# Optimization experiments

Measured on AMD Instinct MI355X. Metric: run time of the kernel, lower is better.

The kernel has to match this reference:

```python
import jax, jax.numpy as jnp
import numpy as np

T, N, E, D, H, L = 8, 50000, 800000, 128, 128, 2


def setup_inputs() -> dict:
    key = jax.random.key(0)
    ks = jax.random.split(key, 16)
    s = 1.0 / np.sqrt(H)  # glorot-ish scale so gates don't saturate
    inp = {
        "x": jax.random.normal(ks[0], (T, N, D), jnp.float32),
        "h0": jax.random.normal(ks[1], (L, N, H), jnp.float32) * 0.1,
        "edge_index": jax.random.randint(ks[2], (2, E), 0, N, jnp.int32),
    }
    for j, n in enumerate(["Wxz", "Whz", "Wxr", "Whr", "Wxh", "Whh"]):
        inp[n] = jax.random.normal(ks[3 + j], (L, H, H), jnp.float32) * s
    for n in ["bxz", "bhz", "bxr", "bhr", "bxh", "bhh"]:
        inp[n] = jnp.zeros((L, H), jnp.float32)
    return inp


def reference(x, h0, Wxz, Whz, Wxr, Whr, Wxh, Whh,
              bxz, bhz, bxr, bhr, bxh, bhh, edge_index):
    n_nodes = x.shape[1]
    n_layer = h0.shape[0]
    # GCNConv(improved=True): add self-loops with weight 2, symmetric norm.
    loop = jnp.arange(n_nodes, dtype=edge_index.dtype)
    row = jnp.concatenate([edge_index[0], loop])
    col = jnp.concatenate([edge_index[1], loop])
    w = jnp.concatenate([jnp.ones((edge_index.shape[1],), x.dtype),
                         jnp.full((n_nodes,), 2.0, x.dtype)])
    deg = jax.ops.segment_sum(w, row, num_segments=n_nodes)
    dinv = jnp.where(deg > 0, deg ** -0.5, 0.0)
    norm = dinv[row] * w * dinv[col]  # [E+N]

    def gcn(v, W, b):
        # gather -> weight -> scatter-add (identity activation inside GRU)
        m = norm[:, None] * (v @ W)[col]          # [E+N, H]
        return jax.ops.segment_sum(m, row, num_segments=n_nodes) + b

    def step(h, xt):
        hs = []
        inp = xt
        for i in range(n_layer):
            z = jax.nn.sigmoid(gcn(inp, Wxz[i], bxz[i]) + gcn(h[i], Whz[i], bhz[i]))
            r = jax.nn.sigmoid(gcn(inp, Wxr[i], bxr[i]) + gcn(h[i], Whr[i], bhr[i]))
            h_tilde = jnp.tanh(gcn(inp, Wxh[i], bxh[i]) + gcn(r * h[i], Whh[i], bhh[i]))
            hn = z * h[i] + (1.0 - z) * h_tilde
            hs.append(hn)
            inp = hn
        h_new = jnp.stack(hs)
        return h_new, h_new[-1]

    _, hs_top = jax.lax.scan(step, h0, x)  # [T, N, H] top-layer states
    return hs_top
```

## Files before the change

kernel.cpp:

```cpp
#include <hip/hip_runtime.h>
#include <hip/hip_fp16.h>

#define TT 8
#define NN 50000
#define EE 800000
#define HH 128
#define LL 2

typedef __attribute__((ext_vector_type(8))) short short8_t;
typedef __attribute__((ext_vector_type(4))) float f32x4;

__device__ __forceinline__ float bf2f(unsigned short b){ return __uint_as_float(((unsigned)b)<<16); }
__device__ __forceinline__ unsigned short f2bf(float f){
  unsigned u = __float_as_uint(f);
  u += 0x7fffu + ((u>>16)&1u);
  return (unsigned short)(u>>16);
}
__device__ __forceinline__ float fin(float v){
  return (v == v && fabsf(v) < 1e30f) ? v : 0.0f;
}
__device__ __forceinline__ float sigm(float x){ return 1.0f/(1.0f+__expf(-x)); }
__device__ __forceinline__ float tanh_fast(float x){
  float t = __expf(-2.0f*fabsf(x));
  float r = (1.0f-t)/(1.0f+t);
  return copysignf(r,x);
}

__global__ void k_detect(const unsigned short* __restrict__ xr, int* __restrict__ flag){
  __shared__ int sm[256];
  int bad = 0;
  for (int i = threadIdx.x; i < 4096; i += 256){
    float v = bf2f(xr[i]);
    if (!(fabsf(v) < 64.0f)) bad++;
  }
  sm[threadIdx.x] = bad; __syncthreads();
  for (int off=128; off>0; off>>=1){
    if (threadIdx.x < off) sm[threadIdx.x] += sm[threadIdx.x+off];
    __syncthreads();
  }
  if (threadIdx.x == 0) flag[0] = (sm[0] > 8) ? 1 : 0;
}

__global__ void k_hist(const int* __restrict__ row, int* __restrict__ counts, int E){
  int e = blockIdx.x*256 + threadIdx.x;
  if (e < E){
    int r = row[e];
    if ((unsigned)r < (unsigned)NN) atomicAdd(&counts[r], 1);
  }
}
__global__ void k_dinv(const int* __restrict__ counts, float* __restrict__ dinv, int N){
  int i = blockIdx.x*256 + threadIdx.x;
  if (i < N) dinv[i] = rsqrtf((float)counts[i] + 2.0f);
}
__global__ void k_reduce(const int* __restrict__ counts, int* __restrict__ part, int N){
  __shared__ int sm[256];
  int i = blockIdx.x*256 + threadIdx.x;
  sm[threadIdx.x] = (i < N) ? counts[i] : 0;
  __syncthreads();
  for (int off=128; off>0; off>>=1){
    if (threadIdx.x < off) sm[threadIdx.x] += sm[threadIdx.x+off];
    __syncthreads();
  }
  if (threadIdx.x == 0) part[blockIdx.x] = sm[0];
}
__global__ void k_scan_partials(const int* __restrict__ part, int* __restrict__ pscan,
                                int nb, int* __restrict__ rowptr, int N, int E){
  __shared__ int sm[256];
  int t = threadIdx.x;
  int v = (t < nb) ? part[t] : 0;
  sm[t] = v; __syncthreads();
  for (int off=1; off<256; off<<=1){
    int x = (t >= off) ? sm[t-off] : 0;
    __syncthreads();
    sm[t] += x;
    __syncthreads();
  }
  if (t < nb) pscan[t] = sm[t] - v;
  if (t == 0) rowptr[N] = E;
}
__global__ void k_scan_final(const int* __restrict__ counts, const int* __restrict__ pscan,
                             int* __restrict__ rowptr, int* __restrict__ cursor, int N){
  __shared__ int sm[256];
  int t = threadIdx.x;
  int i = blockIdx.x*256 + t;
  int v = (i < N) ? counts[i] : 0;
  sm[t] = v; __syncthreads();
  for (int off=1; off<256; off<<=1){
    int x = (t >= off) ? sm[t-off] : 0;
    __syncthreads();
    sm[t] += x;
    __syncthreads();
  }
  int ex = sm[t] - v + pscan[blockIdx.x];
  if (i < N){ rowptr[i] = ex; cursor[i] = ex; }
}
__global__ void k_fill(const int* __restrict__ row, const int* __restrict__ col,
                       int* __restrict__ cursor, const float* __restrict__ dinv,
                       int* __restrict__ colss, float* __restrict__ wsrc, int E){
  int e = blockIdx.x*256 + threadIdx.x;
  if (e < E){
    int r = row[e];
    if ((unsigned)r >= (unsigned)NN) return;
    int p = atomicAdd(&cursor[r], 1);
    if ((unsigned)p >= (unsigned)EE) return;
    int c = col[e];
    if ((unsigned)c >= (unsigned)NN) c = 0;
    colss[p] = c;
    wsrc[p] = dinv[c];
  }
}
__global__ void k_h0(const void* __restrict__ h0, float* __restrict__ h,
                     const int* __restrict__ flag, int n){
  const int fl = *flag;
  int i = blockIdx.x*256 + threadIdx.x;
  if (i < n){
    float v = fl ? ((const float*)h0)[i] : bf2f(((const unsigned short*)h0)[i]);
    h[i] = fin(v);
  }
}
__global__ void k_transpose(const void* W0, const void* W1, const void* W2,
                            const void* W3, const void* W4, const void* W5,
                            unsigned short* __restrict__ Wt_hi,
                            unsigned short* __restrict__ Wt_lo,
                            const int* __restrict__ flag){
  const int fl = *flag;
  int mat = blockIdx.y;
  int wsel = mat >> 1, l = mat & 1;
  const void* W;
  switch (wsel){
    case 0: W = W0; break; case 1: W = W1; break; case 2: W = W2; break;
    case 3: W = W3; break; case 4: W = W4; break; default: W = W5; break;
  }
  int idx = blockIdx.x*256 + threadIdx.x;
  int n = idx >> 7, k = idx & 127;
  size_t src = (size_t)l*16384 + (size_t)k*128 + n;
  float v = fl ? ((const float*)W)[src] : bf2f(((const unsigned short*)W)[src]);
  v = fin(v);
  unsigned short hi = f2bf(v);
  unsigned short lo = f2bf(v - bf2f(hi));
  Wt_hi[(size_t)mat*16384 + idx] = hi;
  Wt_lo[(size_t)mat*16384 + idx] = lo;
}

__global__ __launch_bounds__(256) void gemm_zr(
    const void* __restrict__ S1, long s1_off, int s1_is_x,
    const float* __restrict__ S2,
    const unsigned short* __restrict__ Wz0, const unsigned short* __restrict__ Wz1,
    const unsigned short* __restrict__ Wz2, const unsigned short* __restrict__ Wz3,
    const unsigned short* __restrict__ Wr0, const unsigned short* __restrict__ Wr1,
    const unsigned short* __restrict__ Wr2, const unsigned short* __restrict__ Wr3,
    __half* __restrict__ Cz, __half* __restrict__ Cr,
    int M, const int* __restrict__ flag)
{
  __shared__ short Alds[128*72];
  __shared__ short Bz[128*72];
  __shared__ short Br[128*72];
  const int fl = *flag;
  const int s1bf = s1_is_x && !fl;
  const int nit = fl ? 16 : 8;
  const int tid = threadIdx.x;
  const int m0 = blockIdx.x * 128;

  const int lane = tid & 63;
  const int wid  = tid >> 6;
  const int wm = (wid & 1) << 6;
  const int wn = (wid >> 1) << 6;
  const int lrow = lane & 15;
  const int lk   = (lane >> 4) << 3;

  f32x4 az[4][4], ar[4][4];
#pragma unroll
  for (int i=0;i<4;++i)
#pragma unroll
    for (int j=0;j<4;++j){ az[i][j] = f32x4{0.f,0.f,0.f,0.f}; ar[i][j] = f32x4{0.f,0.f,0.f,0.f}; }

  const int mrow = tid >> 1;
  const int hf   = tid & 1;
  int arow_g = m0 + mrow; if (arow_g >= M) arow_g = M-1;

  for (int it=0; it<nit; ++it){
    const int phase = it >> 2;
    const int k0 = (it & 3) * 32;
    const int koff = k0 + hf*16;
    const bool useS1 = (phase & 1) == 0;
    {
      unsigned pk[16];
      if (useS1 && s1bf){
        const unsigned short* sp = (const unsigned short*)S1 + s1_off + (size_t)arow_g*HH + koff;
        __align__(16) unsigned short tmp[16];
        *(uint4*)&tmp[0] = ((const uint4*)sp)[0];
        *(uint4*)&tmp[8] = ((const uint4*)sp)[1];
#pragma unroll
        for (int j=0;j<16;++j){
          unsigned short t = tmp[j];
          if ((t & 0x7F80u) == 0x7F80u) t = 0;
          pk[j] = (unsigned)t;
        }
      } else {
        __align__(16) float f[16];
        if (useS1){
          const float* sp = (const float*)S1 + s1_off + (size_t)arow_g*HH + koff;
          *(float4*)&f[0]  = ((const float4*)sp)[0];
          *(float4*)&f[4]  = ((const float4*)sp)[1];
          *(float4*)&f[8]  = ((const float4*)sp)[2];
          *(float4*)&f[12] = ((const float4*)sp)[3];
        } else {
          const float* sp = S2 + (size_t)arow_g*HH + koff;
          *(float4*)&f[0]  = ((const float4*)sp)[0];
          *(float4*)&f[4]  = ((const float4*)sp)[1];
          *(float4*)&f[8]  = ((const float4*)sp)[2];
          *(float4*)&f[12] = ((const float4*)sp)[3];
        }
#pragma unroll
        for (int j=0;j<16;++j){
          float v = fin(f[j]);
          unsigned short hi = f2bf(v);
          unsigned short lo = f2bf(v - bf2f(hi));
          pk[j] = (unsigned)hi | ((unsigned)lo << 16);
        }
      }
      short* arp = &Alds[mrow*72 + hf*32];
#pragma unroll
      for (int q=0;q<4;++q){
        uint4 v; v.x=pk[q*4+0]; v.y=pk[q*4+1]; v.z=pk[q*4+2]; v.w=pk[q*4+3];
        *(uint4*)(void*)(arp + q*8) = v;
      }
    }
    {
      const unsigned short* wz = (phase==0) ? Wz0 : (phase==1) ? Wz1 : (phase==2) ? Wz2 : Wz3;
      const unsigned short* wr = (phase==0) ? Wr0 : (phase==1) ? Wr1 : (phase==2) ? Wr2 : Wr3;
      const unsigned short* wpz = wz + (size_t)mrow*HH + koff;
      const unsigned short* wpr = wr + (size_t)mrow*HH + koff;
      __align__(16) unsigned short tz[16], tr[16];
      *(uint4*)&tz[0] = ((const uint4*)wpz)[0];
      *(uint4*)&tz[8] = ((const uint4*)wpz)[1];
      *(uint4*)&tr[0] = ((const uint4*)wpr)[0];
      *(uint4*)&tr[8] = ((const uint4*)wpr)[1];
      short* bzp = &Bz[mrow*72 + hf*32];
      short* brp = &Br[mrow*72 + hf*32];
#pragma unroll
      for (int q=0;q<4;++q){
        uint4 vz, vr;
        vz.x = ((unsigned)tz[q*4+0])*0x00010001u; vz.y = ((unsigned)tz[q*4+1])*0x00010001u;
        vz.z = ((unsigned)tz[q*4+2])*0x00010001u; vz.w = ((unsigned)tz[q*4+3])*0x00010001u;
        vr.x = ((unsigned)tr[q*4+0])*0x00010001u; vr.y = ((unsigned)tr[q*4+1])*0x00010001u;
        vr.z = ((unsigned)tr[q*4+2])*0x00010001u; vr.w = ((unsigned)tr[q*4+3])*0x00010001u;
        *(uint4*)(void*)(bzp + q*8) = vz;
        *(uint4*)(void*)(brp + q*8) = vr;
      }
    }
    __syncthreads();
#pragma unroll
    for (int ks=0; ks<2; ++ks){
      short8_t af[4], bz[4], br[4];
#pragma unroll
      for (int mt=0;mt<4;++mt)
        af[mt] = *(const short8_t*)&Alds[(wm + mt*16 + lrow)*72 + ks*32 + lk];
#pragma unroll
      for (int nt=0;nt<4;++nt){
        bz[nt] = *(const short8_t*)&Bz[(wn + nt*16 + lrow)*72 + ks*32 + lk];
        br[nt] = *(const short8_t*)&Br[(wn + nt*16 + lrow)*72 + ks*32 + lk];
      }
#pragma unroll
      for (int mt=0;mt<4;++mt)
#pragma unroll
        for (int nt=0;nt<4;++nt){
          az[mt][nt] = __builtin_amdgcn_mfma_f32_16x16x32_bf16(af[mt], bz[nt], az[mt][nt], 0, 0, 0);
          ar[mt][nt] = __builtin_amdgcn_mfma_f32_16x16x32_bf16(af[mt], br[nt], ar[mt][nt], 0, 0, 0);
        }
    }
    __syncthreads();
  }
#pragma unroll
  for (int mt=0;mt<4;++mt){
    int rbase = m0 + wm + mt*16 + ((lane>>4)<<2);
#pragma unroll
    for (int nt=0;nt<4;++nt){
      int cc = wn + nt*16 + (lane & 15);
      f32x4 vz = az[mt][nt];
      f32x4 vr = ar[mt][nt];
#pragma unroll
      for (int r=0;r<4;++r){
        int row = rbase + r;
        if (row < M){
          Cz[(size_t)row*HH + cc] = __float2half_rn(vz[r]);
          Cr[(size_t)row*HH + cc] = __float2half_rn(vr[r]);
        }
      }
    }
  }
}

__global__ __launch_bounds__(256) void gemm_h(
    const void* __restrict__ S1, long s1_off, int s1_is_x,
    const __half* __restrict__ S2,
    const unsigned short* __restrict__ W0, const unsigned short* __restrict__ W1,
    const unsigned short* __restrict__ W2, const unsigned short* __restrict__ W3,
    __half* __restrict__ C, int M, const int* __restrict__ flag)
{
  __shared__ short Alds[128*72];
  __shared__ short Blds[128*72];
  const int fl = *flag;
  const int s1bf = s1_is_x && !fl;
  const int nit = fl ? 16 : 8;
  const int tid = threadIdx.x;
  const int m0 = blockIdx.x * 128;

  const int lane = tid & 63;
  const int wid  = tid >> 6;
  const int wm = (wid & 1) << 6;
  const int wn = (wid >> 1) << 6;
  const int lrow = lane & 15;
  const int lk   = (lane >> 4) << 3;

  f32x4 acc[4][4];
#pragma unroll
  for (int i=0;i<4;++i)
#pragma unroll
    for (int j=0;j<4;++j) acc[i][j] = f32x4{0.f,0.f,0.f,0.f};

  const int mrow = tid >> 1;
  const int hf = tid & 1;
  int arow_g = m0 + mrow; if (arow_g >= M) arow_g = M-1;

  for (int it=0; it<nit; ++it){
    const int phase = it >> 2;
    const int k0 = (it & 3) * 32;
    const int koff = k0 + hf*16;
    const bool useS1 = (phase & 1) == 0;
    {
      unsigned pk[16];
      if (useS1 && s1bf){
        const unsigned short* sp = (const unsigned short*)S1 + s1_off + (size_t)arow_g*HH + koff;
        __align__(16) unsigned short tmp[16];
        *(uint4*)&tmp[0] = ((const uint4*)sp)[0];
        *(uint4*)&tmp[8] = ((const uint4*)sp)[1];
#pragma unroll
        for (int j=0;j<16;++j){
          unsigned short t = tmp[j];
          if ((t & 0x7F80u) == 0x7F80u) t = 0;
          pk[j] = (unsigned)t;
        }
      } else {
        __align__(16) float f[16];
        if (useS1){
          const float* sp = (const float*)S1 + s1_off + (size_t)arow_g*HH + koff;
          *(float4*)&f[0]  = ((const float4*)sp)[0];
          *(float4*)&f[4]  = ((const float4*)sp)[1];
          *(float4*)&f[8]  = ((const float4*)sp)[2];
          *(float4*)&f[12] = ((const float4*)sp)[3];
        } else {
          const __half* sp = S2 + (size_t)arow_g*HH + koff;
          __align__(16) __half tmp[16];
          *(uint4*)&tmp[0] = ((const uint4*)sp)[0];
          *(uint4*)&tmp[8] = ((const uint4*)sp)[1];
#pragma unroll
          for (int j=0;j<16;++j) f[j] = __half2float(tmp[j]);
        }
#pragma unroll
        for (int j=0;j<16;++j){
          float v = fin(f[j]);
          unsigned short hi = f2bf(v);
          unsigned short lo = f2bf(v - bf2f(hi));
          pk[j] = (unsigned)hi | ((unsigned)lo << 16);
        }
      }
      short* arp = &Alds[mrow*72 + hf*32];
#pragma unroll
      for (int q=0;q<4;++q){
        uint4 v; v.x=pk[q*4+0]; v.y=pk[q*4+1]; v.z=pk[q*4+2]; v.w=pk[q*4+3];
        *(uint4*)(void*)(arp + q*8) = v;
      }
    }
    {
      const unsigned short* wb = (phase==0) ? W0 : (phase==1) ? W1 : (phase==2) ? W2 : W3;
      const unsigned short* wp = wb + (size_t)mrow*HH + koff;
      __align__(16) unsigned short tb[16];
      *(uint4*)&tb[0] = ((const uint4*)wp)[0];
      *(uint4*)&tb[8] = ((const uint4*)wp)[1];
      unsigned pb[16];
#pragma unroll
      for (int j=0;j<16;++j) pb[j] = ((unsigned)tb[j]) * 0x00010001u;
      short* brp = &Blds[mrow*72 + hf*32];
#pragma unroll
      for (int q=0;q<4;++q){
        uint4 v; v.x=pb[q*4+0]; v.y=pb[q*4+1]; v.z=pb[q*4+2]; v.w=pb[q*4+3];
        *(uint4*)(void*)(brp + q*8) = v;
      }
    }
    __syncthreads();
#pragma unroll
    for (int ks=0; ks<2; ++ks){
      short8_t af[4], bfr[4];
#pragma unroll
      for (int mt=0;mt<4;++mt)
        af[mt] = *(const short8_t*)&Alds[(wm + mt*16 + lrow)*72 + ks*32 + lk];
#pragma unroll
      for (int nt=0;nt<4;++nt)
        bfr[nt] = *(const short8_t*)&Blds[(wn + nt*16 + lrow)*72 + ks*32 + lk];
#pragma unroll
      for (int mt=0;mt<4;++mt)
#pragma unroll
        for (int nt=0;nt<4;++nt)
          acc[mt][nt] = __builtin_amdgcn_mfma_f32_16x16x32_bf16(af[mt], bfr[nt], acc[mt][nt], 0, 0, 0);
    }
    __syncthreads();
  }
#pragma unroll
  for (int mt=0;mt<4;++mt){
    int rbase = m0 + wm + mt*16 + ((lane>>4)<<2);
#pragma unroll
    for (int nt=0;nt<4;++nt){
      int cc = wn + nt*16 + (lane & 15);
      f32x4 a = acc[mt][nt];
#pragma unroll
      for (int r=0;r<4;++r){
        int row = rbase + r;
        if (row < M) C[(size_t)row*HH + cc] = __float2half_rn(a[r]);
      }
    }
  }
}

__global__ __launch_bounds__(256) void prop_zr(
    const __half* __restrict__ Uz, const __half* __restrict__ Ur,
    const int* __restrict__ rowptr, const int* __restrict__ cols,
    const float* __restrict__ wsrc, const float* __restrict__ dinv,
    const void* __restrict__ bxz, const void* __restrict__ bhz,
    const void* __restrict__ bxr, const void* __restrict__ bhr, int boff,
    const float* __restrict__ hl, __half2* __restrict__ zbuf,
    __half2* __restrict__ rhbuf, const int* __restrict__ flag, int N)
{
  const int fl = *flag;
  int lane = threadIdx.x & 63;
  int d = (blockIdx.x << 2) + (threadIdx.x >> 6);
  if (d >= N) return;
  float di = dinv[d];
  const __half2* Uz2 = (const __half2*)Uz;
  const __half2* Ur2 = (const __half2*)Ur;
  float2 az = __half22float2(Uz2[(size_t)d*64 + lane]);
  float2 ar = __half22float2(Ur2[(size_t)d*64 + lane]);
  float sw = 2.0f*di;
  az.x *= sw; az.y *= sw; ar.x *= sw; ar.y *= sw;
  int b = rowptr[d], e = rowptr[d+1];
  if (b < 0) b = 0; if (e > EE) e = EE; if (e < b) e = b;
  for (int base=b; base<e; base+=64){
    int cnt = e - base; if (cnt > 64) cnt = 64;
    int idx = base + lane;
    int mc = (idx < e) ? cols[idx] : 0;
    float mw = (idx < e) ? wsrc[idx] : 0.0f;
    if ((unsigned)mc >= (unsigned)NN){ mc = 0; mw = 0.0f; }
    for (int j=0;j<cnt;++j){
      int s = __shfl(mc, j);
      float w = __shfl(mw, j);
      float2 vz = __half22float2(Uz2[(size_t)s*64 + lane]);
      float2 vr = __half22float2(Ur2[(size_t)s*64 + lane]);
      az.x += w*vz.x; az.y += w*vz.y;
      ar.x += w*vr.x; ar.y += w*vr.y;
    }
  }
  int c = boff + (lane << 1);
  float bxz0 = fl ? ((const float*)bxz)[c]   : bf2f(((const unsigned short*)bxz)[c]);
  float bxz1 = fl ? ((const float*)bxz)[c+1] : bf2f(((const unsigned short*)bxz)[c+1]);
  float bhz0 = fl ? ((const float*)bhz)[c]   : bf2f(((const unsigned short*)bhz)[c]);
  float bhz1 = fl ? ((const float*)bhz)[c+1] : bf2f(((const unsigned short*)bhz)[c+1]);
  float bxr0 = fl ? ((const float*)bxr)[c]   : bf2f(((const unsigned short*)bxr)[c]);
  float bxr1 = fl ? ((const float*)bxr)[c+1] : bf2f(((const unsigned short*)bxr)[c+1]);
  float bhr0 = fl ? ((const float*)bhr)[c]   : bf2f(((const unsigned short*)bhr)[c]);
  float bhr1 = fl ? ((const float*)bhr)[c+1] : bf2f(((const unsigned short*)bhr)[c+1]);
  float z0 = sigm(di*az.x + fin(bxz0) + fin(bhz0));
  float z1 = sigm(di*az.y + fin(bxz1) + fin(bhz1));
  float r0 = sigm(di*ar.x + fin(bxr0) + fin(bhr0));
  float r1 = sigm(di*ar.y + fin(bxr1) + fin(bhr1));
  float2 hv = ((const float2*)hl)[(size_t)d*64 + lane];
  __half2 oz; oz.x = __float2half_rn(z0); oz.y = __float2half_rn(z1);
  __half2 orh; orh.x = __float2half_rn(r0*hv.x); orh.y = __float2half_rn(r1*hv.y);
  zbuf[(size_t)d*64 + lane] = oz;
  rhbuf[(size_t)d*64 + lane] = orh;
}

__global__ __launch_bounds__(256) void prop_h(
    const __half* __restrict__ U, const int* __restrict__ rowptr,
    const int* __restrict__ cols, const float* __restrict__ wsrc,
    const float* __restrict__ dinv,
    const void* __restrict__ bx, const void* __restrict__ bh, int boff,
    const __half2* __restrict__ zbuf, float* __restrict__ hl,
    void* __restrict__ outbase, long out_off, int has_out,
    const int* __restrict__ flag, int N)
{
  const int fl = *flag;
  int lane = threadIdx.x & 63;
  int d = (blockIdx.x << 2) + (threadIdx.x >> 6);
  if (d >= N) return;
  float di = dinv[d];
  const __half2* U2 = (const __half2*)U;
  float2 a = __half22float2(U2[(size_t)d*64 + lane]);
  float sw = 2.0f*di;
  a.x *= sw; a.y *= sw;
  int b = rowptr[d], e = rowptr[d+1];
  if (b < 0) b = 0; if (e > EE) e = EE; if (e < b) e = b;
  for (int base=b; base<e; base+=64){
    int cnt = e - base; if (cnt > 64) cnt = 64;
    int idx = base + lane;
    int mc = (idx < e) ? cols[idx] : 0;
    float mw = (idx < e) ? wsrc[idx] : 0.0f;
    if ((unsigned)mc >= (unsigned)NN){ mc = 0; mw = 0.0f; }
    for (int j=0;j<cnt;++j){
      int s = __shfl(mc, j);
      float w = __shfl(mw, j);
      float2 v = __half22float2(U2[(size_t)s*64 + lane]);
      a.x += w*v.x; a.y += w*v.y;
    }
  }
  int c = boff + (lane << 1);
  float bx0 = fl ? ((const float*)bx)[c]   : bf2f(((const unsigned short*)bx)[c]);
  float bx1 = fl ? ((const float*)bx)[c+1] : bf2f(((const unsigned short*)bx)[c+1]);
  float bh0 = fl ? ((const float*)bh)[c]   : bf2f(((const unsigned short*)bh)[c]);
  float bh1 = fl ? ((const float*)bh)[c+1] : bf2f(((const unsigned short*)bh)[c+1]);
  float ht0 = tanh_fast(di*a.x + fin(bx0) + fin(bh0));
  float ht1 = tanh_fast(di*a.y + fin(bx1) + fin(bh1));
  __half2 zv2 = zbuf[(size_t)d*64 + lane];
  float z0 = __half2float(zv2.x), z1 = __half2float(zv2.y);
  float2 hv = ((const float2*)hl)[(size_t)d*64 + lane];
  float hn0 = z0*hv.x + (1.0f - z0)*ht0;
  float hn1 = z1*hv.y + (1.0f - z1)*ht1;
  ((float2*)hl)[(size_t)d*64 + lane] = float2{hn0, hn1};
  if (has_out){
    if (fl){
      float* op = (float*)outbase + out_off;
      ((float2*)op)[(size_t)d*64 + lane] = float2{hn0, hn1};
    } else {
      unsigned short* op = (unsigned short*)outbase + out_off;
      ((unsigned int*)op)[(size_t)d*64 + lane] =
          (unsigned)f2bf(hn0) | ((unsigned)f2bf(hn1) << 16);
    }
  }
}

extern "C" void kernel_launch(void* const* d_in, const int* in_sizes, int n_in,
                              void* d_out, int out_size, void* d_ws, size_t ws_size,
                              hipStream_t stream)
{
  const void* x  = d_in[0];
  const void* h0 = d_in[1];
  const int* ei  = (const int*)d_in[2];
  const void* Wm[6] = { d_in[3], d_in[4], d_in[5], d_in[6], d_in[7], d_in[8] };
  const void* bxz = d_in[9];
  const void* bhz = d_in[10];
  const void* bxr = d_in[11];
  const void* bhr = d_in[12];
  const void* bxh = d_in[13];
  const void* bhh = d_in[14];

  char* wp_ = (char*)d_ws;
  auto alloc = [&](size_t b)->char*{ char* p = wp_; wp_ += (b + 255) & ~(size_t)255; return p; };
  int*   flag  = (int*)alloc(256);
  float* dinv  = (float*)alloc((size_t)NN*4);
  int*   counts= (int*)alloc((size_t)NN*4);
  int*   rowptr= (int*)alloc((size_t)(NN+1)*4);
  int*   cursor= (int*)alloc((size_t)NN*4);
  int*   part  = (int*)alloc(1024);
  int*   pscan = (int*)alloc(1024);
  int*   colss = (int*)alloc((size_t)EE*4);
  float* wsrc  = (float*)alloc((size_t)EE*4);
  unsigned short* Wt_hi = (unsigned short*)alloc((size_t)12*16384*2);
  unsigned short* Wt_lo = (unsigned short*)alloc((size_t)12*16384*2);
  float*   h     = (float*)alloc((size_t)LL*NN*HH*4);
  __half*  Uz    = (__half*)alloc((size_t)NN*HH*2);
  __half*  Ur    = (__half*)alloc((size_t)NN*HH*2);
  __half*  Uh    = (__half*)alloc((size_t)NN*HH*2);
  __half2* zbuf  = (__half2*)alloc((size_t)NN*HH*2);
  __half2* rhbuf = (__half2*)alloc((size_t)NN*HH*2);

  k_detect<<<1, 256, 0, stream>>>((const unsigned short*)x, flag);
  hipMemsetAsync(counts, 0, (size_t)NN*4, stream);
  hipMemsetAsync(colss, 0, (size_t)EE*4, stream);
  hipMemsetAsync(wsrc,  0, (size_t)EE*4, stream);
  k_hist<<<(EE+255)/256, 256, 0, stream>>>(ei, counts, EE);
  k_dinv<<<(NN+255)/256, 256, 0, stream>>>(counts, dinv, NN);
  k_reduce<<<196, 256, 0, stream>>>(counts, part, NN);
  k_scan_partials<<<1, 256, 0, stream>>>(part, pscan, 196, rowptr, NN, EE);
  k_scan_final<<<196, 256, 0, stream>>>(counts, pscan, rowptr, cursor, NN);
  k_fill<<<(EE+255)/256, 256, 0, stream>>>(ei, ei+EE, cursor, dinv, colss, wsrc, EE);
  k_h0<<<(LL*NN*HH+255)/256, 256, 0, stream>>>(h0, h, flag, LL*NN*HH);
  k_transpose<<<dim3(64,12), 256, 0, stream>>>(Wm[0],Wm[1],Wm[2],Wm[3],Wm[4],Wm[5],
                                               Wt_hi, Wt_lo, flag);

  const int gx = (NN + 127) / 128;
  const int pg = NN / 4;
  for (int t=0; t<TT; ++t){
    for (int l=0; l<LL; ++l){
      const void* S1 = (l==0) ? x : (const void*)h;
      long s1_off = (l==0) ? (long)t*NN*HH : 0;
      int s1_is_x = (l==0) ? 1 : 0;
      float* hl = h + (size_t)l*NN*HH;
      gemm_zr<<<gx, 256, 0, stream>>>(S1, s1_off, s1_is_x, hl,
          Wt_hi + (0*2+l)*16384, Wt_hi + (1*2+l)*16384,
          Wt_lo + (0*2+l)*16384, Wt_lo + (1*2+l)*16384,
          Wt_hi + (2*2+l)*16384, Wt_hi + (3*2+l)*16384,
          Wt_lo + (2*2+l)*16384, Wt_lo + (3*2+l)*16384,
          Uz, Ur, NN, flag);
      prop_zr<<<pg, 256, 0, stream>>>(Uz, Ur, rowptr, colss, wsrc, dinv,
          bxz, bhz, bxr, bhr, l*HH, hl, zbuf, rhbuf, flag, NN);
      gemm_h<<<gx, 256, 0, stream>>>(S1, s1_off, s1_is_x, (const __half*)rhbuf,
          Wt_hi + (4*2+l)*16384, Wt_hi + (5*2+l)*16384,
          Wt_lo + (4*2+l)*16384, Wt_lo + (5*2+l)*16384, Uh, NN, flag);
      prop_h<<<pg, 256, 0, stream>>>(Uh, rowptr, colss, wsrc, dinv,
          bxh, bhh, l*HH, zbuf, hl,
          d_out, (long)t*NN*HH, (l==LL-1) ? 1 : 0, flag, NN);
    }
  }
}
```

Measured before the change: 4.198 ms.

## Interleave z/r projections and edge data, unroll neighbor gathers for memory parallelism

The z and r GEMM outputs now go into one interleaved [N,256] half buffer, so each neighbor gather in prop_zr is a single 8-byte load per lane instead of two 4-byte loads from separate arrays. Column index and source weight are packed into one int2 edge array. The neighbor loops in prop_zr and prop_h are unrolled by 4 and 8 so more independent gathers are in flight. The epilogue splits the wave in half, one half computing z and the other r, which adds a divergent branch and more register pressure.

```diff
diff --git a/kernel.cpp b/kernel.cpp
--- a/kernel.cpp
+++ b/kernel.cpp
@@ -24,6 +24,19 @@
   float t = __expf(-2.0f*fabsf(x));
   float r = (1.0f-t)/(1.0f+t);
   return copysignf(r,x);
+}
+__device__ __forceinline__ float4 up4(uint2 v){
+  __half2 a = *(__half2*)&v.x, b = *(__half2*)&v.y;
+  float2 fa = __half22float2(a), fb = __half22float2(b);
+  return float4{fa.x, fa.y, fb.x, fb.y};
+}
+__device__ __forceinline__ float2 up2(unsigned v){
+  __half2 a = *(__half2*)&v;
+  return __half22float2(a);
+}
+__device__ __forceinline__ unsigned packh2(float a, float b){
+  __half2 h; h.x = __float2half_rn(a); h.y = __float2half_rn(b);
+  return *(unsigned*)&h;
 }
 
 __global__ void k_detect(const unsigned short* __restrict__ xr, int* __restrict__ flag){
@@ -96,7 +109,7 @@
 }
 __global__ void k_fill(const int* __restrict__ row, const int* __restrict__ col,
                        int* __restrict__ cursor, const float* __restrict__ dinv,
-                       int* __restrict__ colss, float* __restrict__ wsrc, int E){
+                       int2* __restrict__ ew, int E){
   int e = blockIdx.x*256 + threadIdx.x;
   if (e < E){
     int r = row[e];
@@ -105,8 +118,7 @@
     if ((unsigned)p >= (unsigned)EE) return;
     int c = col[e];
     if ((unsigned)c >= (unsigned)NN) c = 0;
-    colss[p] = c;
-    wsrc[p] = dinv[c];
+    ew[p] = make_int2(c, __float_as_int(dinv[c]));
   }
 }
 __global__ void k_h0(const void* __restrict__ h0, float* __restrict__ h,
@@ -149,7 +161,7 @@
     const unsigned short* __restrict__ Wz2, const unsigned short* __restrict__ Wz3,
     const unsigned short* __restrict__ Wr0, const unsigned short* __restrict__ Wr1,
     const unsigned short* __restrict__ Wr2, const unsigned short* __restrict__ Wr3,
-    __half* __restrict__ Cz, __half* __restrict__ Cr,
+    __half* __restrict__ Uzr,
     int M, const int* __restrict__ flag)
 {
   __shared__ short Alds[128*72];
@@ -283,8 +295,8 @@
       for (int r=0;r<4;++r){
         int row = rbase + r;
         if (row < M){
-          Cz[(size_t)row*HH + cc] = __float2half_rn(vz[r]);
-          Cr[(size_t)row*HH + cc] = __float2half_rn(vr[r]);
+          Uzr[(size_t)row*256 + cc]       = __float2half_rn(vz[r]);
+          Uzr[(size_t)row*256 + 128 + cc] = __float2half_rn(vr[r]);
         }
       }
     }
@@ -423,9 +435,9 @@
 }
 
 __global__ __launch_bounds__(256) void prop_zr(
-    const __half* __restrict__ Uz, const __half* __restrict__ Ur,
-    const int* __restrict__ rowptr, const int* __restrict__ cols,
-    const float* __restrict__ wsrc, const float* __restrict__ dinv,
+    const __half* __restrict__ Uzr,
+    const int* __restrict__ rowptr, const int2* __restrict__ ew,
+    const float* __restrict__ dinv,
     const void* __restrict__ bxz, const void* __restrict__ bhz,
     const void* __restrict__ bxr, const void* __restrict__ bhr, int boff,
     const float* __restrict__ hl, __half2* __restrict__ zbuf,
@@ -436,53 +448,81 @@
   int d = (blockIdx.x << 2) + (threadIdx.x >> 6);
   if (d >= N) return;
   float di = dinv[d];
-  const __half2* Uz2 = (const __half2*)Uz;
-  const __half2* Ur2 = (const __half2*)Ur;
-  float2 az = __half22float2(Uz2[(size_t)d*64 + lane]);
-  float2 ar = __half22float2(Ur2[(size_t)d*64 + lane]);
+  const uint2* U2 = (const uint2*)Uzr;
+  uint2 sv = U2[(size_t)d*64 + lane];
+  float4 sf = up4(sv);
   float sw = 2.0f*di;
-  az.x *= sw; az.y *= sw; ar.x *= sw; ar.y *= sw;
+  float4 a = float4{sw*sf.x, sw*sf.y, sw*sf.z, sw*sf.w};
   int b = rowptr[d], e = rowptr[d+1];
   if (b < 0) b = 0; if (e > EE) e = EE; if (e < b) e = b;
   for (int base=b; base<e; base+=64){
     int cnt = e - base; if (cnt > 64) cnt = 64;
     int idx = base + lane;
-    int mc = (idx < e) ? cols[idx] : 0;
-    float mw = (idx < e) ? wsrc[idx] : 0.0f;
+    int2 ev = (idx < e) ? ew[idx] : make_int2(0,0);
+    int mc = ev.x; float mw = __int_as_float(ev.y);
     if ((unsigned)mc >= (unsigned)NN){ mc = 0; mw = 0.0f; }
-    for (int j=0;j<cnt;++j){
+    int j = 0;
+    for (; j+3 < cnt; j += 4){
+      int s0 = __shfl(mc, j),   s1 = __shfl(mc, j+1);
+      int s2 = __shfl(mc, j+2), s3 = __shfl(mc, j+3);
+      float w0 = __shfl(mw, j),   w1 = __shfl(mw, j+1);
+      float w2 = __shfl(mw, j+2), w3 = __shfl(mw, j+3);
+      uint2 v0 = U2[(size_t)s0*64 + lane];
+      uint2 v1 = U2[(size_t)s1*64 + lane];
+      uint2 v2 = U2[(size_t)s2*64 + lane];
+      uint2 v3 = U2[(size_t)s3*64 + lane];
+      float4 g0 = up4(v0), g1 = up4(v1), g2 = up4(v2), g3 = up4(v3);
+      a.x += w0*g0.x; a.y += w0*g0.y; a.z += w0*g0.z; a.w += w0*g0.w;
+      a.x += w1*g1.x; a.y += w1*g1.y; a.z += w1*g1.z; a.w += w1*g1.w;
+      a.x += w2*g2.x; a.y += w2*g2.y; a.z += w2*g2.z; a.w += w2*g2.w;
+      a.x += w3*g3.x; a.y += w3*g3.y; a.z += w3*g3.z; a.w += w3*g3.w;
+    }
+    for (; j < cnt; ++j){
       int s = __shfl(mc, j);
       float w = __shfl(mw, j);
-      float2 vz = __half22float2(Uz2[(size_t)s*64 + lane]);
-      float2 vr = __half22float2(Ur2[(size_t)s*64 + lane]);
-      az.x += w*vz.x; az.y += w*vz.y;
-      ar.x += w*vr.x; ar.y += w*vr.y;
-    }
-  }
-  int c = boff + (lane << 1);
-  float bxz0 = fl ? ((const float*)bxz)[c]   : bf2f(((const unsigned short*)bxz)[c]);
-  float bxz1 = fl ? ((const float*)bxz)[c+1] : bf2f(((const unsigned short*)bxz)[c+1]);
-  float bhz0 = fl ? ((const float*)bhz)[c]   : bf2f(((const unsigned short*)bhz)[c]);
-  float bhz1 = fl ? ((const float*)bhz)[c+1] : bf2f(((const unsigned short*)bhz)[c+1]);
-  float bxr0 = fl ? ((const float*)bxr)[c]   : bf2f(((const unsigned short*)bxr)[c]);
-  float bxr1 = fl ? ((const float*)bxr)[c+1] : bf2f(((const unsigned short*)bxr)[c+1]);
-  float bhr0 = fl ? ((const float*)bhr)[c]   : bf2f(((const unsigned short*)bhr)[c]);
-  float bhr1 = fl ? ((const float*)bhr)[c+1] : bf2f(((const unsigned short*)bhr)[c+1]);
-  float z0 = sigm(di*az.x + fin(bxz0) + fin(bhz0));
-  float z1 = sigm(di*az.y + fin(bxz1) + fin(bhz1));
-  float r0 = sigm(di*ar.x + fin(bxr0) + fin(bhr0));
-  float r1 = sigm(di*ar.y + fin(bxr1) + fin(bhr1));
-  float2 hv = ((const float2*)hl)[(size_t)d*64 + lane];
-  __half2 oz; oz.x = __float2half_rn(z0); oz.y = __float2half_rn(z1);
-  __half2 orh; orh.x = __float2half_rn(r0*hv.x); orh.y = __float2half_rn(r1*hv.y);
-  zbuf[(size_t)d*64 + lane] = oz;
-  rhbuf[(size_t)d*64 + lane] = orh;
+      float4 g = up4(U2[(size_t)s*64 + lane]);
+      a.x += w*g.x; a.y += w*g.y; a.z += w*g.z; a.w += w*g.w;
+    }
+  }
+  int l5 = lane & 31;
+  int c = boff + (l5 << 2);
+  if (lane < 32){
+    float bz0 = fl ? ((const float*)bxz)[c+0] : bf2f(((const unsigned short*)bxz)[c+0]);
+    float bz1 = fl ? ((const float*)bxz)[c+1] : bf2f(((const unsigned short*)bxz)[c+1]);
+    float bz2 = fl ? ((const float*)bxz)[c+2] : bf2f(((const unsigned short*)bxz)[c+2]);
+    float bz3 = fl ? ((const float*)bxz)[c+3] : bf2f(((const unsigned short*)bxz)[c+3]);
+    float hz0 = fl ? ((const float*)bhz)[c+0] : bf2f(((const unsigned short*)bhz)[c+0]);
+    float hz1 = fl ? ((const float*)bhz)[c+1] : bf2f(((const unsigned short*)bhz)[c+1]);
+    float hz2 = fl ? ((const float*)bhz)[c+2] : bf2f(((const unsigned short*)bhz)[c+2]);
+    float hz3 = fl ? ((const float*)bhz)[c+3] : bf2f(((const unsigned short*)bhz)[c+3]);
+    float g0 = sigm(di*a.x + fin(bz0) + fin(hz0));
+    float g1 = sigm(di*a.y + fin(bz1) + fin(hz1));
+    float g2 = sigm(di*a.z + fin(bz2) + fin(hz2));
+    float g3 = sigm(di*a.w + fin(bz3) + fin(hz3));
+    uint2 o; o.x = packh2(g0, g1); o.y = packh2(g2, g3);
+    ((uint2*)zbuf)[(size_t)d*32 + l5] = o;
+  } else {
+    float br0 = fl ? ((const float*)bxr)[c+0] : bf2f(((const unsigned short*)bxr)[c+0]);
+    float br1 = fl ? ((const float*)bxr)[c+1] : bf2f(((const unsigned short*)bxr)[c+1]);
+    float br2 = fl ? ((const float*)bxr)[c+2] : bf2f(((const unsigned short*)bxr)[c+2]);
+    float br3 = fl ? ((const float*)bxr)[c+3] : bf2f(((const unsigned short*)bxr)[c+3]);
+    float hr0 = fl ? ((const float*)bhr)[c+0] : bf2f(((const unsigned short*)bhr)[c+0]);
+    float hr1 = fl ? ((const float*)bhr)[c+1] : bf2f(((const unsigned short*)bhr)[c+1]);
+    float hr2 = fl ? ((const float*)bhr)[c+2] : bf2f(((const unsigned short*)bhr)[c+2]);
+    float hr3 = fl ? ((const float*)bhr)[c+3] : bf2f(((const unsigned short*)bhr)[c+3]);
+    float r0 = sigm(di*a.x + fin(br0) + fin(hr0));
+    float r1 = sigm(di*a.y + fin(br1) + fin(hr1));
+    float r2 = sigm(di*a.z + fin(br2) + fin(hr2));
+    float r3 = sigm(di*a.w + fin(br3) + fin(hr3));
+    float4 hv = ((const float4*)hl)[(size_t)d*32 + l5];
+    uint2 o; o.x = packh2(r0*hv.x, r1*hv.y); o.y = packh2(r2*hv.z, r3*hv.w);
+    ((uint2*)rhbuf)[(size_t)d*32 + l5] = o;
+  }
 }
 
 __global__ __launch_bounds__(256) void prop_h(
     const __half* __restrict__ U, const int* __restrict__ rowptr,
-    const int* __restrict__ cols, const float* __restrict__ wsrc,
-    const float* __restrict__ dinv,
+    const int2* __restrict__ ew, const float* __restrict__ dinv,
     const void* __restrict__ bx, const void* __restrict__ bh, int boff,
     const __half2* __restrict__ zbuf, float* __restrict__ hl,
     void* __restrict__ outbase, long out_off, int has_out,
@@ -493,23 +533,52 @@
   int d = (blockIdx.x << 2) + (threadIdx.x >> 6);
   if (d >= N) return;
   float di = dinv[d];
-  const __half2* U2 = (const __half2*)U;
-  float2 a = __half22float2(U2[(size_t)d*64 + lane]);
+  const unsigned* U1 = (const unsigned*)U;
+  float2 sf = up2(U1[(size_t)d*64 + lane]);
   float sw = 2.0f*di;
-  a.x *= sw; a.y *= sw;
+  float2 a = float2{sw*sf.x, sw*sf.y};
   int b = rowptr[d], e = rowptr[d+1];
   if (b < 0) b = 0; if (e > EE) e = EE; if (e < b) e = b;
   for (int base=b; base<e; base+=64){
     int cnt = e - base; if (cnt > 64) cnt = 64;
     int idx = base + lane;
-    int mc = (idx < e) ? cols[idx] : 0;
-    float mw = (idx < e) ? wsrc[idx] : 0.0f;
+    int2 ev = (idx < e) ? ew[idx] : make_int2(0,0);
+    int mc = ev.x; float mw = __int_as_float(ev.y);
     if ((unsigned)mc >= (unsigned)NN){ mc = 0; mw = 0.0f; }
-    for (int j=0;j<cnt;++j){
+    int j = 0;
+    for (; j+7 < cnt; j += 8){
+      int s0 = __shfl(mc, j),   s1 = __shfl(mc, j+1);
+      int s2 = __shfl(mc, j+2), s3 = __shfl(mc, j+3);
+      int s4 = __shfl(mc, j+4), s5 = __shfl(mc, j+5);
+      int s6 = __shfl(mc, j+6), s7 = __shfl(mc, j+7);
+      float w0 = __shfl(mw, j),   w1 = __shfl(mw, j+1);
+      float w2 = __shfl(mw, j+2), w3 = __shfl(mw, j+3);
+      float w4 = __shfl(mw, j+4), w5 = __shfl(mw, j+5);
+      float w6 = __shfl(mw, j+6), w7 = __shfl(mw, j+7);
+      unsigned v0 = U1[(size_t)s0*64 + lane];
+      unsigned v1 = U1[(size_t)s1*64 + lane];
+      unsigned v2 = U1[(size_t)s2*64 + lane];
+      unsigned v3 = U1[(size_t)s3*64 + lane];
+      unsigned v4 = U1[(size_t)s4*64 + lane];
+      unsigned v5 = U1[(size_t)s5*64 + lane];
+      unsigned v6 = U1[(size_t)s6*64 + lane];
+      unsigned v7 = U1[(size_t)s7*64 + lane];
+      float2 g0 = up2(v0), g1 = up2(v1), g2 = up2(v2), g3 = up2(v3);
+      float2 g4 = up2(v4), g5 = up2(v5), g6 = up2(v6), g7 = up2(v7);
+      a.x += w0*g0.x; a.y += w0*g0.y;
+      a.x += w1*g1.x; a.y += w1*g1.y;
+      a.x += w2*g2.x; a.y += w2*g2.y;
+      a.x += w3*g3.x; a.y += w3*g3.y;
+      a.x += w4*g4.x; a.y += w4*g4.y;
+      a.x += w5*g5.x; a.y += w5*g5.y;
+      a.x += w6*g6.x; a.y += w6*g6.y;
+      a.x += w7*g7.x; a.y += w7*g7.y;
+    }
+    for (; j < cnt; ++j){
       int s = __shfl(mc, j);
       float w = __shfl(mw, j);
-      float2 v = __half22float2(U2[(size_t)s*64 + lane]);
-      a.x += w*v.x; a.y += w*v.y;
+      float2 g = up2(U1[(size_t)s*64 + lane]);
+      a.x += w*g.x; a.y += w*g.y;
     }
   }
   int c = boff + (lane << 1);
@@ -561,27 +630,24 @@
   int*   cursor= (int*)alloc((size_t)NN*4);
   int*   part  = (int*)alloc(1024);
   int*   pscan = (int*)alloc(1024);
-  int*   colss = (int*)alloc((size_t)EE*4);
-  float* wsrc  = (float*)alloc((size_t)EE*4);
+  int2*  ew    = (int2*)alloc((size_t)EE*8);
   unsigned short* Wt_hi = (unsigned short*)alloc((size_t)12*16384*2);
   unsigned short* Wt_lo = (unsigned short*)alloc((size_t)12*16384*2);
   float*   h     = (float*)alloc((size_t)LL*NN*HH*4);
-  __half*  Uz    = (__half*)alloc((size_t)NN*HH*2);
-  __half*  Ur    = (__half*)alloc((size_t)NN*HH*2);
+  __half*  Uzr   = (__half*)alloc((size_t)NN*256*2);
   __half*  Uh    = (__half*)alloc((size_t)NN*HH*2);
   __half2* zbuf  = (__half2*)alloc((size_t)NN*HH*2);
   __half2* rhbuf = (__half2*)alloc((size_t)NN*HH*2);
 
   k_detect<<<1, 256, 0, stream>>>((const unsigned short*)x, flag);
   hipMemsetAsync(counts, 0, (size_t)NN*4, stream);
-  hipMemsetAsync(colss, 0, (size_t)EE*4, stream);
-  hipMemsetAsync(wsrc,  0, (size_t)EE*4, stream);
+  hipMemsetAsync(ew, 0, (size_t)EE*8, stream);
   k_hist<<<(EE+255)/256, 256, 0, stream>>>(ei, counts, EE);
   k_dinv<<<(NN+255)/256, 256, 0, stream>>>(counts, dinv, NN);
   k_reduce<<<196, 256, 0, stream>>>(counts, part, NN);
   k_scan_partials<<<1, 256, 0, stream>>>(part, pscan, 196, rowptr, NN, EE);
   k_scan_final<<<196, 256, 0, stream>>>(counts, pscan, rowptr, cursor, NN);
-  k_fill<<<(EE+255)/256, 256, 0, stream>>>(ei, ei+EE, cursor, dinv, colss, wsrc, EE);
+  k_fill<<<(EE+255)/256, 256, 0, stream>>>(ei, ei+EE, cursor, dinv, ew, EE);
   k_h0<<<(LL*NN*HH+255)/256, 256, 0, stream>>>(h0, h, flag, LL*NN*HH);
   k_transpose<<<dim3(64,12), 256, 0, stream>>>(Wm[0],Wm[1],Wm[2],Wm[3],Wm[4],Wm[5],
                                                Wt_hi, Wt_lo, flag);
@@ -599,13 +665,13 @@
           Wt_lo + (0*2+l)*16384, Wt_lo + (1*2+l)*16384,
           Wt_hi + (2*2+l)*16384, Wt_hi + (3*2+l)*16384,
           Wt_lo + (2*2+l)*16384, Wt_lo + (3*2+l)*16384,
-          Uz, Ur, NN, flag);
-      prop_zr<<<pg, 256, 0, stream>>>(Uz, Ur, rowptr, colss, wsrc, dinv,
+          Uzr, NN, flag);
+      prop_zr<<<pg, 256, 0, stream>>>(Uzr, rowptr, ew, dinv,
           bxz, bhz, bxr, bhr, l*HH, hl, zbuf, rhbuf, flag, NN);
       gemm_h<<<gx, 256, 0, stream>>>(S1, s1_off, s1_is_x, (const __half*)rhbuf,
           Wt_hi + (4*2+l)*16384, Wt_hi + (5*2+l)*16384,
           Wt_lo + (4*2+l)*16384, Wt_lo + (5*2+l)*16384, Uh, NN, flag);
-      prop_h<<<pg, 256, 0, stream>>>(Uh, rowptr, colss, wsrc, dinv,
+      prop_h<<<pg, 256, 0, stream>>>(Uh, rowptr, ew, dinv,
           bxh, bhh, l*HH, zbuf, hl,
           d_out, (long)t*NN*HH, (l==LL-1) ? 1 : 0, flag, NN);
     }
```

New measurement: 3.805 ms. 1.1x faster.
